# Performance work log

Hardware: AMD Instinct MI355X
Metric: run time of the kernel (lower is better)

## Reference

```python
import jax, jax.numpy as jnp
import numpy as np

WS = 7          # window size (square)
SHIFT = 3       # shift size
NH = 8          # num heads
DIM = 256
B, H, W = 32, 56, 56


def _relative_position_index(ws: int) -> np.ndarray:
    coords = np.stack(np.meshgrid(np.arange(ws), np.arange(ws), indexing='ij'))  # (2, ws, ws)
    cf = coords.reshape(2, -1)                                                   # (2, N)
    rel = cf[:, :, None] - cf[:, None, :]                                        # (2, N, N)
    rel = rel.transpose(1, 2, 0).copy()
    rel[:, :, 0] += ws - 1
    rel[:, :, 1] += ws - 1
    rel[:, :, 0] *= 2 * ws - 1
    return rel.sum(-1).reshape(-1).astype(np.int32)                              # (N*N,)


def _shift_mask(h: int, w: int, ws: int, shift: int) -> np.ndarray:
    img = np.zeros((h, w), dtype=np.float32)
    cnt = 0
    for hs in ((0, -ws), (-ws, -shift), (-shift, None)):
        for wsl in ((0, -ws), (-ws, -shift), (-shift, None)):
            img[hs[0]:hs[1], wsl[0]:wsl[1]] = cnt
            cnt += 1
    nwh, nww = h // ws, w // ws
    m = img.reshape(nwh, ws, nww, ws).transpose(0, 2, 1, 3).reshape(nwh * nww, ws * ws)
    am = m[:, None, :] - m[:, :, None]                 # (nW, N, N)
    return np.where(am != 0, np.float32(-100.0), np.float32(0.0))


def setup_inputs() -> dict:
    key = jax.random.key(0)
    ks = jax.random.split(key, 5)
    x = jax.random.normal(ks[0], (B, H, W, DIM), jnp.float32)
    qkv_weight = jax.random.normal(ks[1], (3 * DIM, DIM), jnp.float32) * 0.02
    qkv_bias = jnp.zeros((3 * DIM,), jnp.float32)
    proj_weight = jax.random.normal(ks[2], (DIM, DIM), jnp.float32) * 0.02
    proj_bias = jnp.zeros((DIM,), jnp.float32)
    rel_bias_table = jax.random.normal(ks[3], ((2 * WS - 1) ** 2, NH), jnp.float32) * 0.02
    rel_pos_index = jnp.asarray(_relative_position_index(WS))
    return {
        'x': x, 'qkv_weight': qkv_weight, 'qkv_bias': qkv_bias,
        'proj_weight': proj_weight, 'proj_bias': proj_bias,
        'rel_bias_table': rel_bias_table, 'rel_pos_index': rel_pos_index,
    }


def reference(x, qkv_weight, qkv_bias, proj_weight, proj_bias, rel_bias_table, rel_pos_index):
    b, h, w, c = x.shape
    n = WS * WS
    hd = c // NH
    nwh, nww = h // WS, w // WS
    nw = nwh * nww

    # relative position bias: (1, NH, N, N)
    bias = rel_bias_table[rel_pos_index].reshape(n, n, NH).transpose(2, 0, 1)[None]

    # cyclic shift
    xs = jnp.roll(x, (-SHIFT, -SHIFT), axis=(1, 2))

    # window partition -> (B*nW, N, C)
    xw = xs.reshape(b, nwh, WS, nww, WS, c).transpose(0, 1, 3, 2, 4, 5).reshape(b * nw, n, c)

    qkv = xw @ qkv_weight.T + qkv_bias
    qkv = qkv.reshape(b * nw, n, 3, NH, hd).transpose(2, 0, 3, 1, 4)  # (3, B*nW, NH, N, hd)
    q = qkv[0] * (hd ** -0.5)
    k = qkv[1]
    v = qkv[2]

    attn = jnp.einsum('bhnd,bhmd->bhnm', q, k) + bias                # (B*nW, NH, N, N)

    # shift mask (static)
    amask = jnp.asarray(_shift_mask(h, w, WS, SHIFT))                # (nW, N, N)
    attn = attn.reshape(b, nw, NH, n, n) + amask[None, :, None]
    attn = jax.nn.softmax(attn.reshape(b * nw, NH, n, n), axis=-1)

    out = jnp.einsum('bhnm,bhmd->bhnd', attn, v)                     # (B*nW, NH, N, hd)
    out = out.transpose(0, 2, 1, 3).reshape(b * nw, n, c)
    out = out @ proj_weight.T + proj_bias

    # window reverse + reverse shift
    out = out.reshape(b, nwh, nww, WS, WS, c).transpose(0, 1, 3, 2, 4, 5).reshape(b, h, w, c)
    out = jnp.roll(out, (SHIFT, SHIFT), axis=(1, 2))
    return out
```

## Files before the change

kernel.cpp:

```cpp
#include <hip/hip_runtime.h>
#include <hip/hip_bf16.h>


#define NTOK 49
#define DIM_ 256
#define NH_  8
#define NQKV 196608
#define NPRJ 65536
#define NTABP 131072

#define WSP_B  393216ull
#define TAB_B  524288ull
#define NEED_TAB (TAB_B + (unsigned long long)NTABP * 4)

typedef short v8s __attribute__((ext_vector_type(8)));
typedef float v4f __attribute__((ext_vector_type(4)));
typedef float v16f __attribute__((ext_vector_type(16)));

#define MFMA16 __builtin_amdgcn_mfma_f32_16x16x32_bf16
#define MFMA32 __builtin_amdgcn_mfma_f32_32x32x16_bf16
#define LGKM_WAIT() asm volatile("s_waitcnt lgkmcnt(0)" ::: "memory")

static __device__ __forceinline__ v8s zero_v8s() {
    v8s z = {0, 0, 0, 0, 0, 0, 0, 0};
    return z;
}

static __device__ __forceinline__ v16f zero_v16f() {
    v16f z;
    #pragma unroll
    for (int i = 0; i < 16; ++i) z[i] = 0.0f;
    return z;
}

static __device__ __forceinline__ v8s lds_frag(const __hip_bfloat16* p, int row,
                                               int stride, int koff, int nrows) {
    if (row < nrows) return *(const v8s*)(p + row * stride + koff);
    return zero_v8s();
}

static __device__ __forceinline__ v8s cvt8(const float* p) {
    v4f a = *(const v4f*)p;
    v4f b = *(const v4f*)(p + 4);
    union { v8s v; __hip_bfloat16 h[8]; } r;
    r.h[0] = __float2bfloat16(a[0]); r.h[1] = __float2bfloat16(a[1]);
    r.h[2] = __float2bfloat16(a[2]); r.h[3] = __float2bfloat16(a[3]);
    r.h[4] = __float2bfloat16(b[0]); r.h[5] = __float2bfloat16(b[1]);
    r.h[6] = __float2bfloat16(b[2]); r.h[7] = __float2bfloat16(b[3]);
    return r.v;
}

__global__ __launch_bounds__(256) void prep_kernel(
    const float* __restrict__ qkvW, const float* __restrict__ projW,
    const float* __restrict__ rbt, const int* __restrict__ rpi,
    __hip_bfloat16* __restrict__ wsQ, __hip_bfloat16* __restrict__ wsP,
    float* __restrict__ tabP, int doTab)
{
    int i = blockIdx.x * 256 + threadIdx.x;
    if (i < NQKV) { wsQ[i] = __float2bfloat16(qkvW[i]); return; }
    int j = i - NQKV;
    if (j < NPRJ) { wsP[j] = __float2bfloat16(projW[j]); return; }
    int t = j - NPRJ;
    if (!doTab || t >= NTABP) return;
    int cls = t >> 15;
    int rem = t & 32767;
    int h = rem >> 12;
    int p = rem & 4095;
    int row = p >> 6, col = p & 63;
    float val = -1e30f;
    if (row < NTOK && col < NTOK) {
        int rh = (cls & 1) ? (((row / 7) < 4) ? 1 : 2) : 0;
        int rw = (cls & 2) ? (((row % 7) < 4) ? 1 : 2) : 0;
        int ch = (cls & 1) ? (((col / 7) < 4) ? 1 : 2) : 0;
        int cw = (cls & 2) ? (((col % 7) < 4) ? 1 : 2) : 0;
        float mask = ((rh * 3 + rw) != (ch * 3 + cw)) ? -100.0f : 0.0f;
        val = rbt[rpi[row * 49 + col] * NH_ + h] + mask;
    }
    tabP[t] = val;
}

__global__ __launch_bounds__(256) void swin_mega_kernel(
    const float* __restrict__ x,
    const float* __restrict__ qkvB,
    const __hip_bfloat16* __restrict__ wsQ,
    const __hip_bfloat16* __restrict__ wsP,
    const float* __restrict__ projB,
    const float* __restrict__ tabP,
    float* __restrict__ out)
{
    constexpr int SXS = 264;
    constexpr int QKS = 40;
    constexpr int VTS = 72;
    constexpr int PS  = 72;
    constexpr int WVSZ = 2 * NTOK * QKS + 32 * VTS;

    __shared__ alignas(16) __hip_bfloat16 s_x[NTOK * SXS];
    __shared__ alignas(16) __hip_bfloat16 s_wv[4 * WVSZ];

    const int tid = threadIdx.x, wave = tid >> 6, lane = tid & 63;
    const int quad = lane >> 4, l16 = lane & 15;
    const int l32 = lane & 31, half = lane >> 5;
    const int win = blockIdx.x;
    const int b = win >> 6, wh = (win >> 3) & 7, wwi = win & 7;
    const int cls = ((wh == 7) ? 1 : 0) | ((wwi == 7) ? 2 : 0);

    __hip_bfloat16* wq  = s_wv + wave * WVSZ;
    __hip_bfloat16* wk  = wq + NTOK * QKS;
    __hip_bfloat16* wvt = wq + 2 * NTOK * QKS;
    __hip_bfloat16* wp  = wq;

    for (int i = lane; i < 32 * 7; i += 64)
        wvt[(i / 7) * VTS + 49 + (i % 7)] = __float2bfloat16(0.0f);

    for (int i = tid; i < NTOK * 64; i += 256) {
        int tok = i >> 6, f4 = (i & 63) * 4;
        int r = tok / 7, c = tok - r * 7;
        int hg = wh * 7 + r + 3; if (hg >= 56) hg -= 56;
        int wg = wwi * 7 + c + 3; if (wg >= 56) wg -= 56;
        float4 v = *(const float4*)(x + ((b * 56 + hg) * 56 + wg) * DIM_ + f4);
        union { ushort4 u4; __hip_bfloat16 h[4]; } pkst;
        pkst.h[0] = __float2bfloat16(v.x);
        pkst.h[1] = __float2bfloat16(v.y);
        pkst.h[2] = __float2bfloat16(v.z);
        pkst.h[3] = __float2bfloat16(v.w);
        *(ushort4*)(s_x + tok * SXS + f4) = pkst.u4;
    }
    __syncthreads();

    const float qscale = 0.17677669529663687f;
    const int r1 = (32 + l32 < NTOK) ? (32 + l32) : 0;
    const __hip_bfloat16* arow0 = s_x + l32 * SXS + half * 8;
    const __hip_bfloat16* arow1 = s_x + r1 * SXS + half * 8;

    v4f ohacc[2][4][2];

    #pragma unroll
    for (int hp = 0; hp < 2; ++hp) {
        const int h = wave * 2 + hp;

        #pragma unroll
        for (int m = 0; m < 3; ++m) {
            const int nb = m * 256 + h * 32;
            const __hip_bfloat16* wrow = wsQ + (nb + l32) * DIM_ + half * 8;
            v16f acc0 = zero_v16f(), acc1 = zero_v16f();

            if (m < 2) {
                #pragma unroll
                for (int kh = 0; kh < 2; ++kh) {
                    v8s wf[8];
                    #pragma unroll
                    for (int k = 0; k < 8; ++k)
                        wf[k] = *(const v8s*)(wrow + kh * 128 + k * 16);
                    #pragma unroll
                    for (int k = 0; k < 8; ++k) {
                        v8s a0 = *(const v8s*)(arow0 + kh * 128 + k * 16);
                        v8s a1 = *(const v8s*)(arow1 + kh * 128 + k * 16);
                        acc0 = MFMA32(a0, wf[k], acc0, 0, 0, 0);
                        acc1 = MFMA32(a1, wf[k], acc1, 0, 0, 0);
                    }
                }
                float bias = qkvB[nb + l32];
                float sc = (m == 0) ? qscale : 1.0f;
                __hip_bfloat16* dst = (m == 0) ? wq : wk;
                #pragma unroll
                for (int rg = 0; rg < 16; ++rg) {
                    int rowoff = (rg & 3) + 8 * (rg >> 2) + 4 * half;
                    dst[rowoff * QKS + l32] =
                        __float2bfloat16((acc0[rg] + bias) * sc);
                    int tok1 = 32 + rowoff;
                    if (tok1 < NTOK)
                        dst[tok1 * QKS + l32] =
                            __float2bfloat16((acc1[rg] + bias) * sc);
                }
            } else {
                #pragma unroll
                for (int kh = 0; kh < 2; ++kh) {
                    v8s wf[8];
                    #pragma unroll
                    for (int k = 0; k < 8; ++k)
                        wf[k] = *(const v8s*)(wrow + kh * 128 + k * 16);
                    #pragma unroll
                    for (int k = 0; k < 8; ++k) {
                        v8s b0 = *(const v8s*)(arow0 + kh * 128 + k * 16);
                        v8s b1 = *(const v8s*)(arow1 + kh * 128 + k * 16);
                        acc0 = MFMA32(wf[k], b0, acc0, 0, 0, 0);
                        acc1 = MFMA32(wf[k], b1, acc1, 0, 0, 0);
                    }
                }
                const int tok1 = 32 + l32;
                #pragma unroll
                for (int rg = 0; rg < 16; ++rg) {
                    int feat = (rg & 3) + 8 * (rg >> 2) + 4 * half;
                    float bias = qkvB[nb + feat];
                    wvt[feat * VTS + l32] = __float2bfloat16(acc0[rg] + bias);
                    if (tok1 < NTOK)
                        wvt[feat * VTS + tok1] = __float2bfloat16(acc1[rg] + bias);
                }
            }
        }
        LGKM_WAIT();

        const float* tabh = tabP + (cls * NH_ + h) * 4096;

        v8s qa[4], kb[4];
        #pragma unroll
        for (int mt = 0; mt < 4; ++mt) {
            qa[mt] = lds_frag(wq, mt * 16 + l16, QKS, quad * 8, NTOK);
            kb[mt] = lds_frag(wk, mt * 16 + l16, QKS, quad * 8, NTOK);
        }
        v8s pb[2][2];
        #pragma unroll
        for (int nt = 0; nt < 2; ++nt) {
            const __hip_bfloat16* vr = wvt + (nt * 16 + l16) * VTS;
            pb[nt][0] = *(const v8s*)(vr + quad * 8);
            pb[nt][1] = (quad == 3) ? zero_v8s() : *(const v8s*)(vr + 32 + quad * 8);
        }
        LGKM_WAIT();

        #pragma unroll
        for (int ntq = 0; ntq < 4; ++ntq) {
            const int qtok = ntq * 16 + l16;
            v4f tv[4];
            #pragma unroll
            for (int mt = 0; mt < 4; ++mt)
                tv[mt] = *(const v4f*)(tabh + qtok * 64 + mt * 16 + quad * 4);
            v4f st[4];
            #pragma unroll
            for (int mt = 0; mt < 4; ++mt) {
                v4f z = {0.f, 0.f, 0.f, 0.f};
                st[mt] = MFMA16(kb[mt], qa[ntq], z, 0, 0, 0);
            }
            float v[16];
            float rmax = -1e30f;
            #pragma unroll
            for (int mt = 0; mt < 4; ++mt)
                #pragma unroll
                for (int rg = 0; rg < 4; ++rg) {
                    float s = st[mt][rg] + tv[mt][rg];
                    v[mt * 4 + rg] = s;
                    rmax = fmaxf(rmax, s);
                }
            rmax = fmaxf(rmax, __shfl_xor(rmax, 16, 64));
            rmax = fmaxf(rmax, __shfl_xor(rmax, 32, 64));
            float rsum = 0.f;
            #pragma unroll
            for (int i = 0; i < 16; ++i) {
                float e = (v[i] <= -1e29f) ? 0.f : __expf(v[i] - rmax);
                v[i] = e;
                rsum += e;
            }
            rsum += __shfl_xor(rsum, 16, 64);
            rsum += __shfl_xor(rsum, 32, 64);
            if (qtok < NTOK) {
                float inv = 1.0f / rsum;
                #pragma unroll
                for (int mt = 0; mt < 4; ++mt) {
                    union { __hip_bfloat16 h4[4]; unsigned long long u; } pk;
                    #pragma unroll
                    for (int rg = 0; rg < 4; ++rg)
                        pk.h4[rg] = __float2bfloat16(v[mt * 4 + rg] * inv);
                    *(unsigned long long*)(wp + qtok * PS + mt * 16 + quad * 4) = pk.u;
                }
            }
        }
        LGKM_WAIT();

        #pragma unroll
        for (int mtile = 0; mtile < 4; ++mtile) {
            v8s pa0 = lds_frag(wp, mtile * 16 + l16, PS, quad * 8, NTOK);
            v8s pa1 = lds_frag(wp, mtile * 16 + l16, PS, 32 + quad * 8, NTOK);
            #pragma unroll
            for (int nt = 0; nt < 2; ++nt) {
                v4f z = {0.f, 0.f, 0.f, 0.f};
                v4f acc = MFMA16(pa0, pb[nt][0], z, 0, 0, 0);
                acc = MFMA16(pa1, pb[nt][1], acc, 0, 0, 0);
                ohacc[hp][mtile][nt] = acc;
            }
        }
        LGKM_WAIT();
    }

    __syncthreads();
    __hip_bfloat16* s_o = s_x;

    #pragma unroll
    for (int hp = 0; hp < 2; ++hp) {
        const int h = wave * 2 + hp;
        #pragma unroll
        for (int mtile = 0; mtile < 4; ++mtile)
            #pragma unroll
            for (int nt = 0; nt < 2; ++nt)
                #pragma unroll
                for (int rg = 0; rg < 4; ++rg) {
                    int tok = mtile * 16 + quad * 4 + rg;
                    if (tok < NTOK)
                        s_o[tok * SXS + h * 32 + nt * 16 + l16] =
                            __float2bfloat16(ohacc[hp][mtile][nt][rg]);
                }
    }
    __syncthreads();

    {
        const int m0 = wave * 16;
        v8s af[8];
        #pragma unroll
        for (int ks = 0; ks < 8; ++ks)
            af[ks] = lds_frag(s_o, m0 + l16, SXS, ks * 32 + quad * 8, NTOK);

        int ooff[4];
        #pragma unroll
        for (int rg = 0; rg < 4; ++rg) {
            int row = m0 + quad * 4 + rg;
            if (row < NTOK) {
                int r = row / 7, c = row - r * 7;
                int hg = wh * 7 + r + 3; if (hg >= 56) hg -= 56;
                int wg = wwi * 7 + c + 3; if (wg >= 56) wg -= 56;
                ooff[rg] = ((b * 56 + hg) * 56 + wg) * DIM_;
            } else ooff[rg] = -1;
        }
        LGKM_WAIT();

        #pragma unroll
        for (int t = 0; t < 16; ++t) {
            const __hip_bfloat16* wrow = wsP + (t * 16 + l16) * DIM_;
            v4f acc = {0.f, 0.f, 0.f, 0.f};
            #pragma unroll
            for (int ks = 0; ks < 8; ++ks) {
                v8s wf = *(const v8s*)(wrow + ks * 32 + quad * 8);
                acc = MFMA16(af[ks], wf, acc, 0, 0, 0);
            }
            float pbv = projB[t * 16 + l16];
            #pragma unroll
            for (int rg = 0; rg < 4; ++rg)
                if (ooff[rg] >= 0)
                    out[ooff[rg] + t * 16 + l16] = acc[rg] + pbv;
        }
    }
}

__global__ __launch_bounds__(256, 2) void swin_attn_fused(
    const float* __restrict__ x,
    const float* __restrict__ qkvB,
    const float* __restrict__ projB,
    const float* __restrict__ rbt,
    const int*   __restrict__ rpi,
    const __hip_bfloat16* __restrict__ wsQ,
    const __hip_bfloat16* __restrict__ wsP,
    const float* __restrict__ biasTab,
    float*       __restrict__ out)
{
    constexpr int QKS = 40;
    constexpr int VTS = 72;
    constexpr int PS  = 72;
    constexpr int OS  = 264;
    constexpr int WVSZ = 6224;

    __shared__ alignas(16) __hip_bfloat16 s_wv[4 * WVSZ];
    __shared__ alignas(16) __hip_bfloat16 s_o[NTOK * OS];
    __shared__ int s_off[NTOK];
    __shared__ int s_reg[NTOK];

    const int tid  = threadIdx.x;
    const int wave = tid >> 6;
    const int lane = tid & 63;
    const int quad = lane >> 4;
    const int l16  = lane & 15;

    const int wid  = blockIdx.x;
    const int b    = wid >> 6;
    const int wIdx = wid & 63;
    const int wh   = wIdx >> 3;
    const int wwi  = wIdx & 7;

    if (tid < NTOK) {
        int r = tid / 7, c = tid - r * 7;
        int hs = wh * 7 + r, ws = wwi * 7 + c;
        int hg = hs + 3; if (hg >= 56) hg -= 56;
        int wg = ws + 3; if (wg >= 56) wg -= 56;
        s_off[tid] = ((b * 56 + hg) * 56 + wg) * DIM_;
        int rh = (hs < 49) ? 0 : ((hs < 53) ? 1 : 2);
        int rw = (ws < 49) ? 0 : ((ws < 53) ? 1 : 2);
        s_reg[tid] = rh * 3 + rw;
    }

    __hip_bfloat16* wq  = s_wv + wave * WVSZ;
    __hip_bfloat16* wk  = wq + NTOK * QKS;
    __hip_bfloat16* wvt = wq + 2 * NTOK * QKS;
    __hip_bfloat16* wp  = wq;

    for (int i = lane; i < 32 * 15; i += 64) {
        int f = i / 15, kk = 49 + (i % 15);
        wvt[f * VTS + kk] = __float2bfloat16(0.0f);
    }
    __syncthreads();

    const float qscale = 0.17677669529663687f;

    for (int hp = 0; hp < 2; ++hp) {
        const int h = wave * 2 + hp;
        LGKM_WAIT();

        for (int mh = 0; mh < 2; ++mh) {
            const int mbase = mh * 32;
            v8s at[2][8];
            #pragma unroll
            for (int sub = 0; sub < 2; ++sub) {
                int tok = mbase + sub * 16 + l16;
                const float* xr = (tok < NTOK) ? (x + s_off[tok]) : nullptr;
                #pragma unroll
                for (int ks = 0; ks < 8; ++ks)
                    at[sub][ks] = xr ? cvt8(xr + ks * 32 + quad * 8) : zero_v8s();
            }
            #pragma unroll
            for (int t = 0; t < 6; ++t) {
                int mat = t >> 1, ntile = t & 1;
                int nout = mat * 256 + h * 32 + ntile * 16 + l16;
                const __hip_bfloat16* wrow = wsQ + nout * DIM_;
                v4f a0 = {0.f, 0.f, 0.f, 0.f}, a1 = {0.f, 0.f, 0.f, 0.f};
                #pragma unroll
                for (int ks = 0; ks < 8; ++ks) {
                    v8s bfr = *(const v8s*)(wrow + ks * 32 + quad * 8);
                    a0 = MFMA16(at[0][ks], bfr, a0, 0, 0, 0);
                    a1 = MFMA16(at[1][ks], bfr, a1, 0, 0, 0);
                }
                float bias  = qkvB[nout];
                float scale = (mat == 0) ? qscale : 1.0f;
                #pragma unroll
                for (int sub = 0; sub < 2; ++sub) {
                    v4f acc = sub ? a1 : a0;
                    #pragma unroll
                    for (int rg = 0; rg < 4; ++rg) {
                        int row = mbase + sub * 16 + quad * 4 + rg;
                        if (row < NTOK) {
                            float val = (acc[rg] + bias) * scale;
                            int col = ntile * 16 + l16;
                            __hip_bfloat16 bv = __float2bfloat16(val);
                            if (mat == 0)      wq[row * QKS + col] = bv;
                            else if (mat == 1) wk[row * QKS + col] = bv;
                            else               wvt[col * VTS + row] = bv;
                        }
                    }
                }
            }
        }
        LGKM_WAIT();

        v8s qa[4], kb[4];
        #pragma unroll
        for (int i = 0; i < 4; ++i) {
            qa[i] = lds_frag(wq, i * 16 + l16, QKS, quad * 8, NTOK);
            kb[i] = lds_frag(wk, i * 16 + l16, QKS, quad * 8, NTOK);
        }
        int regc[4];
        #pragma unroll
        for (int nt = 0; nt < 4; ++nt) {
            int col = nt * 16 + l16;
            regc[nt] = (col < NTOK) ? s_reg[col] : -1;
        }
        LGKM_WAIT();
        const float* tabh = biasTab ? (biasTab + h * 4096) : nullptr;
        #pragma unroll
        for (int mtile = 0; mtile < 4; ++mtile) {
            v4f sa[4];
            #pragma unroll
            for (int nt = 0; nt < 4; ++nt) {
                v4f z = {0.f, 0.f, 0.f, 0.f};
                sa[nt] = MFMA16(qa[mtile], kb[nt], z, 0, 0, 0);
            }
            #pragma unroll
            for (int rg = 0; rg < 4; ++rg) {
                int row = mtile * 16 + quad * 4 + rg;
                bool rok = row < NTOK;
                int rr = rok ? s_reg[row] : -2;
                float v[4];
                float rmax = -1e30f;
                #pragma unroll
                for (int nt = 0; nt < 4; ++nt) {
                    int col = nt * 16 + l16;
                    float s = -1e30f;
                    if (rok && col < NTOK) {
                        float bv = tabh ? tabh[row * 64 + col]
                                        : rbt[rpi[row * 49 + col] * NH_ + h];
                        s = sa[nt][rg] + bv;
                        if (rr != regc[nt]) s -= 100.0f;
                    }
                    v[nt] = s;
                    rmax = fmaxf(rmax, s);
                }
                #pragma unroll
                for (int mm = 8; mm >= 1; mm >>= 1)
                    rmax = fmaxf(rmax, __shfl_xor(rmax, mm, 64));
                float rsum = 0.f;
                #pragma unroll
                for (int nt = 0; nt < 4; ++nt) {
                    float e = (v[nt] <= -1e29f) ? 0.f : __expf(v[nt] - rmax);
                    v[nt] = e;
                    rsum += e;
                }
                #pragma unroll
                for (int mm = 8; mm >= 1; mm >>= 1)
                    rsum += __shfl_xor(rsum, mm, 64);
                if (rok) {
                    float inv = 1.0f / rsum;
                    #pragma unroll
                    for (int nt = 0; nt < 4; ++nt)
                        wp[row * PS + nt * 16 + l16] = __float2bfloat16(v[nt] * inv);
                }
            }
        }
        LGKM_WAIT();

        v8s pb[2][2];
        #pragma unroll
        for (int nt = 0; nt < 2; ++nt)
            #pragma unroll
            for (int ks = 0; ks < 2; ++ks)
                pb[nt][ks] = *(const v8s*)(wvt + (nt * 16 + l16) * VTS + ks * 32 + quad * 8);
        #pragma unroll
        for (int mtile = 0; mtile < 4; ++mtile) {
            v8s pa0 = lds_frag(wp, mtile * 16 + l16, PS, quad * 8, NTOK);
            v8s pa1 = lds_frag(wp, mtile * 16 + l16, PS, 32 + quad * 8, NTOK);
            #pragma unroll
            for (int nt = 0; nt < 2; ++nt) {
                v4f z = {0.f, 0.f, 0.f, 0.f};
                v4f acc = MFMA16(pa0, pb[nt][0], z, 0, 0, 0);
                acc = MFMA16(pa1, pb[nt][1], acc, 0, 0, 0);
                #pragma unroll
                for (int rg = 0; rg < 4; ++rg) {
                    int row = mtile * 16 + quad * 4 + rg;
                    if (row < NTOK)
                        s_o[row * OS + h * 32 + nt * 16 + l16] = __float2bfloat16(acc[rg]);
                }
            }
        }
    }
    __syncthreads();

    {
        int m0 = wave * 16;
        v8s af[8];
        #pragma unroll
        for (int ks = 0; ks < 8; ++ks)
            af[ks] = lds_frag(s_o, m0 + l16, OS, ks * 32 + quad * 8, NTOK);
        #pragma unroll
        for (int t = 0; t < 16; ++t) {
            const __hip_bfloat16* wrow = wsP + (t * 16 + l16) * DIM_;
            v4f acc = {0.f, 0.f, 0.f, 0.f};
            #pragma unroll
            for (int ks = 0; ks < 8; ++ks) {
                v8s bfr = *(const v8s*)(wrow + ks * 32 + quad * 8);
                acc = MFMA16(af[ks], bfr, acc, 0, 0, 0);
            }
            float pbv = projB[t * 16 + l16];
            #pragma unroll
            for (int rg = 0; rg < 4; ++rg) {
                int row = m0 + quad * 4 + rg;
                if (row < NTOK)
                    out[s_off[row] + t * 16 + l16] = acc[rg] + pbv;
            }
        }
    }
}

extern "C" void kernel_launch(void* const* d_in, const int* in_sizes, int n_in,
                              void* d_out, int out_size, void* d_ws, size_t ws_size,
                              hipStream_t stream) {
    const float* x     = (const float*)d_in[0];
    const float* qkvW  = (const float*)d_in[1];
    const float* qkvB  = (const float*)d_in[2];
    const float* projW = (const float*)d_in[3];
    const float* projB = (const float*)d_in[4];
    const float* rbt   = (const float*)d_in[5];
    const int*   rpi   = (const int*)d_in[6];
    float* o = (float*)d_out;

    __hip_bfloat16* wsQ = (__hip_bfloat16*)d_ws;
    __hip_bfloat16* wsP = (__hip_bfloat16*)((char*)d_ws + WSP_B);
    float* tabP         = (float*)((char*)d_ws + TAB_B);

    const int prepBlocks = (NQKV + NPRJ + NTABP + 255) / 256;

    if (ws_size >= NEED_TAB) {
        prep_kernel<<<prepBlocks, 256, 0, stream>>>(qkvW, projW, rbt, rpi,
                                                    wsQ, wsP, tabP, 1);
        swin_mega_kernel<<<2048, 256, 0, stream>>>(x, qkvB, wsQ, wsP, projB,
                                                   tabP, o);
    } else {
        prep_kernel<<<prepBlocks, 256, 0, stream>>>(qkvW, projW, rbt, rpi,
                                                    wsQ, wsP, tabP, 0);
        swin_attn_fused<<<2048, 256, 0, stream>>>(x, qkvB, projB, rbt, rpi,
                                                  wsQ, wsP, nullptr, o);
    }
}
```

Before: 437.2 us.

## Shrink per-wave LDS scratch, raise occupancy, split proj GEMM by output columns

Per-wave scratch is reduced to one buffer that is reused in turn for Q, K, V-transposed and P. Q and K fragments are moved into registers right after each is computed, and sched_barrier fences keep the compiler from reordering across the reuse points. The smaller LDS footprint, together with launch_bounds(256,3), targets three blocks per CU. The output projection now gives each wave four column tiles across all rows instead of one row tile across all columns, so each wave loads a quarter of the projection weights but reads more activation fragments from LDS.

```diff
diff --git a/kernel.cpp b/kernel.cpp
--- a/kernel.cpp
+++ b/kernel.cpp
@@ -20,6 +20,11 @@
 #define MFMA16 __builtin_amdgcn_mfma_f32_16x16x32_bf16
 #define MFMA32 __builtin_amdgcn_mfma_f32_32x32x16_bf16
 #define LGKM_WAIT() asm volatile("s_waitcnt lgkmcnt(0)" ::: "memory")
+#define WAVE_FENCE()                                   \
+    do {                                               \
+        asm volatile("s_waitcnt lgkmcnt(0)" ::: "memory"); \
+        __builtin_amdgcn_sched_barrier(0);             \
+    } while (0)
 
 static __device__ __forceinline__ v8s zero_v8s() {
     v8s z = {0, 0, 0, 0, 0, 0, 0, 0};
@@ -79,7 +84,7 @@
     tabP[t] = val;
 }
 
-__global__ __launch_bounds__(256) void swin_mega_kernel(
+__global__ __launch_bounds__(256, 3) void swin_mega_kernel(
     const float* __restrict__ x,
     const float* __restrict__ qkvB,
     const __hip_bfloat16* __restrict__ wsQ,
@@ -90,9 +95,9 @@
 {
     constexpr int SXS = 264;
     constexpr int QKS = 40;
-    constexpr int VTS = 72;
+    constexpr int VTS = 56;
     constexpr int PS  = 72;
-    constexpr int WVSZ = 2 * NTOK * QKS + 32 * VTS;
+    constexpr int WVSZ = NTOK * PS;
 
     __shared__ alignas(16) __hip_bfloat16 s_x[NTOK * SXS];
     __shared__ alignas(16) __hip_bfloat16 s_wv[4 * WVSZ];
@@ -104,13 +109,7 @@
     const int b = win >> 6, wh = (win >> 3) & 7, wwi = win & 7;
     const int cls = ((wh == 7) ? 1 : 0) | ((wwi == 7) ? 2 : 0);
 
-    __hip_bfloat16* wq  = s_wv + wave * WVSZ;
-    __hip_bfloat16* wk  = wq + NTOK * QKS;
-    __hip_bfloat16* wvt = wq + 2 * NTOK * QKS;
-    __hip_bfloat16* wp  = wq;
-
-    for (int i = lane; i < 32 * 7; i += 64)
-        wvt[(i / 7) * VTS + 49 + (i % 7)] = __float2bfloat16(0.0f);
+    __hip_bfloat16* wbuf = s_wv + wave * WVSZ;
 
     for (int i = tid; i < NTOK * 64; i += 256) {
         int tok = i >> 6, f4 = (i & 63) * 4;
@@ -132,91 +131,101 @@
     const __hip_bfloat16* arow0 = s_x + l32 * SXS + half * 8;
     const __hip_bfloat16* arow1 = s_x + r1 * SXS + half * 8;
 
+    auto gemm32 = [&](int nb, bool swapped, v16f& acc0, v16f& acc1) {
+        const __hip_bfloat16* wrow = wsQ + (nb + l32) * DIM_ + half * 8;
+        acc0 = zero_v16f(); acc1 = zero_v16f();
+        #pragma unroll
+        for (int kh = 0; kh < 2; ++kh) {
+            v8s wf[8];
+            #pragma unroll
+            for (int k = 0; k < 8; ++k)
+                wf[k] = *(const v8s*)(wrow + kh * 128 + k * 16);
+            #pragma unroll
+            for (int k = 0; k < 8; ++k) {
+                v8s a0 = *(const v8s*)(arow0 + kh * 128 + k * 16);
+                v8s a1 = *(const v8s*)(arow1 + kh * 128 + k * 16);
+                if (!swapped) {
+                    acc0 = MFMA32(a0, wf[k], acc0, 0, 0, 0);
+                    acc1 = MFMA32(a1, wf[k], acc1, 0, 0, 0);
+                } else {
+                    acc0 = MFMA32(wf[k], a0, acc0, 0, 0, 0);
+                    acc1 = MFMA32(wf[k], a1, acc1, 0, 0, 0);
+                }
+            }
+        }
+    };
+
     v4f ohacc[2][4][2];
 
     #pragma unroll
     for (int hp = 0; hp < 2; ++hp) {
         const int h = wave * 2 + hp;
-
-        #pragma unroll
-        for (int m = 0; m < 3; ++m) {
-            const int nb = m * 256 + h * 32;
-            const __hip_bfloat16* wrow = wsQ + (nb + l32) * DIM_ + half * 8;
-            v16f acc0 = zero_v16f(), acc1 = zero_v16f();
-
-            if (m < 2) {
-                #pragma unroll
-                for (int kh = 0; kh < 2; ++kh) {
-                    v8s wf[8];
-                    #pragma unroll
-                    for (int k = 0; k < 8; ++k)
-                        wf[k] = *(const v8s*)(wrow + kh * 128 + k * 16);
-                    #pragma unroll
-                    for (int k = 0; k < 8; ++k) {
-                        v8s a0 = *(const v8s*)(arow0 + kh * 128 + k * 16);
-                        v8s a1 = *(const v8s*)(arow1 + kh * 128 + k * 16);
-                        acc0 = MFMA32(a0, wf[k], acc0, 0, 0, 0);
-                        acc1 = MFMA32(a1, wf[k], acc1, 0, 0, 0);
-                    }
-                }
-                float bias = qkvB[nb + l32];
-                float sc = (m == 0) ? qscale : 1.0f;
-                __hip_bfloat16* dst = (m == 0) ? wq : wk;
-                #pragma unroll
-                for (int rg = 0; rg < 16; ++rg) {
-                    int rowoff = (rg & 3) + 8 * (rg >> 2) + 4 * half;
-                    dst[rowoff * QKS + l32] =
-                        __float2bfloat16((acc0[rg] + bias) * sc);
-                    int tok1 = 32 + rowoff;
-                    if (tok1 < NTOK)
-                        dst[tok1 * QKS + l32] =
-                            __float2bfloat16((acc1[rg] + bias) * sc);
-                }
-            } else {
-                #pragma unroll
-                for (int kh = 0; kh < 2; ++kh) {
-                    v8s wf[8];
-                    #pragma unroll
-                    for (int k = 0; k < 8; ++k)
-                        wf[k] = *(const v8s*)(wrow + kh * 128 + k * 16);
-                    #pragma unroll
-                    for (int k = 0; k < 8; ++k) {
-                        v8s b0 = *(const v8s*)(arow0 + kh * 128 + k * 16);
-                        v8s b1 = *(const v8s*)(arow1 + kh * 128 + k * 16);
-                        acc0 = MFMA32(wf[k], b0, acc0, 0, 0, 0);
-                        acc1 = MFMA32(wf[k], b1, acc1, 0, 0, 0);
-                    }
-                }
-                const int tok1 = 32 + l32;
-                #pragma unroll
-                for (int rg = 0; rg < 16; ++rg) {
-                    int feat = (rg & 3) + 8 * (rg >> 2) + 4 * half;
-                    float bias = qkvB[nb + feat];
-                    wvt[feat * VTS + l32] = __float2bfloat16(acc0[rg] + bias);
-                    if (tok1 < NTOK)
-                        wvt[feat * VTS + tok1] = __float2bfloat16(acc1[rg] + bias);
-                }
-            }
-        }
-        LGKM_WAIT();
-
-        const float* tabh = tabP + (cls * NH_ + h) * 4096;
-
-        v8s qa[4], kb[4];
-        #pragma unroll
-        for (int mt = 0; mt < 4; ++mt) {
-            qa[mt] = lds_frag(wq, mt * 16 + l16, QKS, quad * 8, NTOK);
-            kb[mt] = lds_frag(wk, mt * 16 + l16, QKS, quad * 8, NTOK);
-        }
-        v8s pb[2][2];
+        v16f acc0, acc1;
+        v8s qa[4], kb[4], pb[2][2];
+
+        gemm32(h * 32, false, acc0, acc1);
+        {
+            float bias = qkvB[h * 32 + l32];
+            #pragma unroll
+            for (int rg = 0; rg < 16; ++rg) {
+                int rowoff = (rg & 3) + 8 * (rg >> 2) + 4 * half;
+                wbuf[rowoff * QKS + l32] =
+                    __float2bfloat16((acc0[rg] + bias) * qscale);
+                int tok1 = 32 + rowoff;
+                if (tok1 < NTOK)
+                    wbuf[tok1 * QKS + l32] =
+                        __float2bfloat16((acc1[rg] + bias) * qscale);
+            }
+        }
+        WAVE_FENCE();
+        #pragma unroll
+        for (int mt = 0; mt < 4; ++mt)
+            qa[mt] = lds_frag(wbuf, mt * 16 + l16, QKS, quad * 8, NTOK);
+        WAVE_FENCE();
+
+        gemm32(256 + h * 32, false, acc0, acc1);
+        {
+            float bias = qkvB[256 + h * 32 + l32];
+            #pragma unroll
+            for (int rg = 0; rg < 16; ++rg) {
+                int rowoff = (rg & 3) + 8 * (rg >> 2) + 4 * half;
+                wbuf[rowoff * QKS + l32] = __float2bfloat16(acc0[rg] + bias);
+                int tok1 = 32 + rowoff;
+                if (tok1 < NTOK)
+                    wbuf[tok1 * QKS + l32] = __float2bfloat16(acc1[rg] + bias);
+            }
+        }
+        WAVE_FENCE();
+        #pragma unroll
+        for (int mt = 0; mt < 4; ++mt)
+            kb[mt] = lds_frag(wbuf, mt * 16 + l16, QKS, quad * 8, NTOK);
+        WAVE_FENCE();
+
+        for (int i = lane; i < 32 * 7; i += 64)
+            wbuf[(i / 7) * VTS + 49 + (i % 7)] = __float2bfloat16(0.0f);
+        gemm32(512 + h * 32, true, acc0, acc1);
+        {
+            const int nb = 512 + h * 32;
+            const int tok1 = 32 + l32;
+            #pragma unroll
+            for (int rg = 0; rg < 16; ++rg) {
+                int feat = (rg & 3) + 8 * (rg >> 2) + 4 * half;
+                float bias = qkvB[nb + feat];
+                wbuf[feat * VTS + l32] = __float2bfloat16(acc0[rg] + bias);
+                if (tok1 < NTOK)
+                    wbuf[feat * VTS + tok1] = __float2bfloat16(acc1[rg] + bias);
+            }
+        }
+        WAVE_FENCE();
         #pragma unroll
         for (int nt = 0; nt < 2; ++nt) {
-            const __hip_bfloat16* vr = wvt + (nt * 16 + l16) * VTS;
+            const __hip_bfloat16* vr = wbuf + (nt * 16 + l16) * VTS;
             pb[nt][0] = *(const v8s*)(vr + quad * 8);
             pb[nt][1] = (quad == 3) ? zero_v8s() : *(const v8s*)(vr + 32 + quad * 8);
         }
-        LGKM_WAIT();
-
+        WAVE_FENCE();
+
+        const float* tabh = tabP + (cls * NH_ + h) * 4096;
         #pragma unroll
         for (int ntq = 0; ntq < 4; ++ntq) {
             const int qtok = ntq * 16 + l16;
@@ -259,16 +268,16 @@
                     #pragma unroll
                     for (int rg = 0; rg < 4; ++rg)
                         pk.h4[rg] = __float2bfloat16(v[mt * 4 + rg] * inv);
-                    *(unsigned long long*)(wp + qtok * PS + mt * 16 + quad * 4) = pk.u;
-                }
-            }
-        }
-        LGKM_WAIT();
+                    *(unsigned long long*)(wbuf + qtok * PS + mt * 16 + quad * 4) = pk.u;
+                }
+            }
+        }
+        WAVE_FENCE();
 
         #pragma unroll
         for (int mtile = 0; mtile < 4; ++mtile) {
-            v8s pa0 = lds_frag(wp, mtile * 16 + l16, PS, quad * 8, NTOK);
-            v8s pa1 = lds_frag(wp, mtile * 16 + l16, PS, 32 + quad * 8, NTOK);
+            v8s pa0 = lds_frag(wbuf, mtile * 16 + l16, PS, quad * 8, NTOK);
+            v8s pa1 = lds_frag(wbuf, mtile * 16 + l16, PS, 32 + quad * 8, NTOK);
             #pragma unroll
             for (int nt = 0; nt < 2; ++nt) {
                 v4f z = {0.f, 0.f, 0.f, 0.f};
@@ -277,7 +286,7 @@
                 ohacc[hp][mtile][nt] = acc;
             }
         }
-        LGKM_WAIT();
+        WAVE_FENCE();
     }
 
     __syncthreads();
@@ -301,39 +310,44 @@
     __syncthreads();
 
     {
-        const int m0 = wave * 16;
-        v8s af[8];
-        #pragma unroll
-        for (int ks = 0; ks < 8; ++ks)
-            af[ks] = lds_frag(s_o, m0 + l16, SXS, ks * 32 + quad * 8, NTOK);
-
-        int ooff[4];
-        #pragma unroll
-        for (int rg = 0; rg < 4; ++rg) {
-            int row = m0 + quad * 4 + rg;
-            if (row < NTOK) {
-                int r = row / 7, c = row - r * 7;
-                int hg = wh * 7 + r + 3; if (hg >= 56) hg -= 56;
-                int wg = wwi * 7 + c + 3; if (wg >= 56) wg -= 56;
-                ooff[rg] = ((b * 56 + hg) * 56 + wg) * DIM_;
-            } else ooff[rg] = -1;
-        }
-        LGKM_WAIT();
-
-        #pragma unroll
-        for (int t = 0; t < 16; ++t) {
+        int ooff[4][4];
+        #pragma unroll
+        for (int mt = 0; mt < 4; ++mt)
+            #pragma unroll
+            for (int rg = 0; rg < 4; ++rg) {
+                int row = mt * 16 + quad * 4 + rg;
+                if (row < NTOK) {
+                    int r = row / 7, c = row - r * 7;
+                    int hg = wh * 7 + r + 3; if (hg >= 56) hg -= 56;
+                    int wg = wwi * 7 + c + 3; if (wg >= 56) wg -= 56;
+                    ooff[mt][rg] = ((b * 56 + hg) * 56 + wg) * DIM_;
+                } else ooff[mt][rg] = -1;
+            }
+
+        #pragma unroll
+        for (int tt = 0; tt < 4; ++tt) {
+            const int t = wave * 4 + tt;
             const __hip_bfloat16* wrow = wsP + (t * 16 + l16) * DIM_;
-            v4f acc = {0.f, 0.f, 0.f, 0.f};
-            #pragma unroll
-            for (int ks = 0; ks < 8; ++ks) {
-                v8s wf = *(const v8s*)(wrow + ks * 32 + quad * 8);
-                acc = MFMA16(af[ks], wf, acc, 0, 0, 0);
-            }
+            v8s wf[8];
+            #pragma unroll
+            for (int ks = 0; ks < 8; ++ks)
+                wf[ks] = *(const v8s*)(wrow + ks * 32 + quad * 8);
             float pbv = projB[t * 16 + l16];
-            #pragma unroll
-            for (int rg = 0; rg < 4; ++rg)
-                if (ooff[rg] >= 0)
-                    out[ooff[rg] + t * 16 + l16] = acc[rg] + pbv;
+
+            #pragma unroll
+            for (int mt = 0; mt < 4; ++mt) {
+                v4f acc = {0.f, 0.f, 0.f, 0.f};
+                #pragma unroll
+                for (int ks = 0; ks < 8; ++ks) {
+                    v8s af = lds_frag(s_o, mt * 16 + l16, SXS,
+                                      ks * 32 + quad * 8, NTOK);
+                    acc = MFMA16(af, wf[ks], acc, 0, 0, 0);
+                }
+                #pragma unroll
+                for (int rg = 0; rg < 4; ++rg)
+                    if (ooff[mt][rg] >= 0)
+                        out[ooff[mt][rg] + t * 16 + l16] = acc[rg] + pbv;
+            }
         }
     }
 }
```

New measurement: 408.4 us. -6.6%, faster.
